# Kernel optimization log

Hardware: AMD Instinct MI355X
Metric: run time of the kernel (lower is better)

## Reference

```python
import jax, jax.numpy as jnp
import numpy as np

B, N, M = 32, 2048, 512
NUM_HEADING_BIN, NUM_SIZE_CLUSTER = 12, 8
OUT_DIM = 3 + 2 * NUM_HEADING_BIN + 4 * NUM_SIZE_CLUSTER  # 59

SPECS = [("sf_w1",64,4),("sf_w2",64,64),("sf_w3",64,64),("sf_w4",128,64),("sf_w5",1024,128),
         ("sh_w1",512,1091),("sh_w2",256,512),("sh_w3",128,256),("sh_w4",128,128),("sh_w5",2,128),
         ("t_w1",128,3),("t_w2",256,128),("t_w3",512,256),("t_fw1",256,515),("t_fw2",128,256),("t_fw3",3,128),
         ("b_w1",128,3),("b_w2",128,128),("b_w3",256,128),("b_w4",512,256),("b_fw1",512,515),("b_fw2",256,512),("b_fw3",OUT_DIM,256)]


def _bn(x, axes):
    # training-mode batch norm, gamma=1 beta=0 (fresh-init torch BatchNorm1d)
    m = jnp.mean(x, axes, keepdims=True)
    v = jnp.var(x, axes, keepdims=True)
    return (x - m) * jax.lax.rsqrt(v + 1e-5)


def _conv(x, w, b):  # 1x1 Conv1d: x (B,C,N), w (O,C), b (O,)
    return jnp.einsum('bcn,oc->bon', x, w) + b[None, :, None]


def _fc(x, w, b):  # x (B,C), w (O,C)
    return x @ w.T + b


def setup_inputs() -> dict:
    key = jax.random.key(0)
    ks = jax.random.split(key, 2 + len(SPECS))
    inp = {}
    inp["point_cloud"] = jax.random.normal(ks[0], (B, N, 4), dtype=jnp.float32)
    cls = jax.random.randint(ks[1], (B,), 0, 3)
    inp["one_hot_vec"] = jax.nn.one_hot(cls, 3, dtype=jnp.float32)
    for i, (nm, o, c) in enumerate(SPECS):
        inp[nm] = jax.random.normal(ks[2 + i], (o, c), dtype=jnp.float32) * (1.0 / np.sqrt(c))
        inp[nm.replace('w', 'b')] = jnp.zeros((o,), jnp.float32)
    return inp


def _forward(point_cloud, one_hot_vec,
             sf_w1, sf_b1, sf_w2, sf_b2, sf_w3, sf_b3, sf_w4, sf_b4, sf_w5, sf_b5,
             sh_w1, sh_b1, sh_w2, sh_b2, sh_w3, sh_b3, sh_w4, sh_b4, sh_w5, sh_b5,
             t_w1, t_b1, t_w2, t_b2, t_w3, t_b3, t_fw1, t_fb1, t_fw2, t_fb2, t_fw3, t_fb3,
             b_w1, b_b1, b_w2, b_b2, b_w3, b_b3, b_w4, b_b4, b_fw1, b_fb1, b_fw2, b_fb2, b_fw3, b_fb3):
    relu = jax.nn.relu
    Bv, Nv = point_cloud.shape[0], point_cloud.shape[1]

    # ---- PointNetSegmentation (PointNetfeat global_feat=False + seg head) ----
    x = point_cloud.transpose(0, 2, 1)                       # (B,4,N)
    h = relu(_bn(_conv(x, sf_w1, sf_b1), (0, 2)))
    pointfeat = relu(_bn(_conv(h, sf_w2, sf_b2), (0, 2)))    # (B,64,N)
    h = relu(_bn(_conv(pointfeat, sf_w3, sf_b3), (0, 2)))
    h = relu(_bn(_conv(h, sf_w4, sf_b4), (0, 2)))
    h = _bn(_conv(h, sf_w5, sf_b5), (0, 2))                  # (B,1024,N), no relu
    g = jnp.max(h, axis=2)                                   # (B,1024)
    g = jnp.concatenate([one_hot_vec, g], axis=1)            # (B,1027)
    feat = jnp.concatenate([jnp.broadcast_to(g[:, :, None], (Bv, 1027, Nv)), pointfeat], axis=1)  # (B,1091,N)
    h = relu(_bn(_conv(feat, sh_w1, sh_b1), (0, 2)))
    h = relu(_bn(_conv(h, sh_w2, sh_b2), (0, 2)))
    h = relu(_bn(_conv(h, sh_w3, sh_b3), (0, 2)))
    h = relu(_bn(_conv(h, sh_w4, sh_b4), (0, 2)))            # dropout p=0.5 -> eval identity
    logits = _conv(h, sh_w5, sh_b5).transpose(0, 2, 1)       # (B,N,2)

    # ---- point_cloud_masking: vectorized mask-select + resample-to-512 ----
    xyz = point_cloud[:, :, :3]
    mask = logits[:, :, 0] < logits[:, :, 1]                 # (B,N) bool
    cnt = jnp.sum(mask, axis=1)                              # (B,)
    mean = jnp.sum(mask[:, :, None] * xyz, axis=1) / jnp.clip(cnt, 1)[:, None].astype(xyz.dtype)
    xyz_c = xyz - mean[:, None, :]                           # centered at mask centroid
    order = jnp.argsort(jnp.logical_not(mask), axis=1, stable=True)  # masked indices first
    u = jax.random.uniform(jax.random.key(42), (Bv, M))
    pos = jnp.minimum((u * cnt[:, None].astype(u.dtype)).astype(jnp.int32),
                      jnp.maximum(cnt[:, None] - 1, 0).astype(jnp.int32))
    idx = jnp.take_along_axis(order, pos, axis=1)            # (B,M) sample w/ replacement from masked set
    object_pc = jnp.take_along_axis(xyz_c, idx[:, :, None], axis=1)  # (B,M,3)
    object_pc = jnp.where(cnt[:, None, None] > 0, object_pc, 0.0)

    x = object_pc.transpose(0, 2, 1)                         # (B,3,M)
    h = relu(_bn(_conv(x, t_w1, t_b1), (0, 2)))
    h = relu(_bn(_conv(h, t_w2, t_b2), (0, 2)))
    h = relu(_bn(_conv(h, t_w3, t_b3), (0, 2)))
    gt = jnp.max(h, axis=2)                                  # (B,512)
    gt = jnp.concatenate([one_hot_vec, gt], axis=1)          # (B,515)
    h = relu(_bn(_fc(gt, t_fw1, t_fb1), 0))
    h = relu(_bn(_fc(h, t_fw2, t_fb2), 0))
    center_delta = _fc(h, t_fw3, t_fb3)                      # (B,3)

    stage1_center = center_delta + mean
    object_pc_new = object_pc - center_delta[:, None, :]

    # ---- PointNet3DboxEstimationNet ----
    x = object_pc_new.transpose(0, 2, 1)                     # (B,3,M)
    h = relu(_bn(_conv(x, b_w1, b_b1), (0, 2)))
    h = relu(_bn(_conv(h, b_w2, b_b2), (0, 2)))
    h = relu(_bn(_conv(h, b_w3, b_b3), (0, 2)))
    h = relu(_bn(_conv(h, b_w4, b_b4), (0, 2)))
    gb = jnp.max(h, axis=2)                                  # (B,512)
    gb = jnp.concatenate([gb, one_hot_vec], axis=1)          # (B,515)
    h = relu(_bn(_fc(gb, b_fw1, b_fb1), 0))
    h = relu(_bn(_fc(h, b_fw2, b_fb2), 0))
    box_out = _fc(h, b_fw3, b_fb3)                           # (B,59)

    center = box_out[:, :3] + stage1_center                  # final box center
    return jnp.concatenate([logits.reshape(Bv, -1), box_out, center], axis=1)  # (B, 2N+59+3)


def reference(point_cloud, one_hot_vec,
              sf_w1, sf_b1, sf_w2, sf_b2, sf_w3, sf_b3, sf_w4, sf_b4, sf_w5, sf_b5,
              sh_w1, sh_b1, sh_w2, sh_b2, sh_w3, sh_b3, sh_w4, sh_b4, sh_w5, sh_b5,
              t_w1, t_b1, t_w2, t_b2, t_w3, t_b3, t_fw1, t_fb1, t_fw2, t_fb2, t_fw3, t_fb3,
              b_w1, b_b1, b_w2, b_b2, b_w3, b_b3, b_w4, b_b4, b_fw1, b_fb1, b_fw2, b_fb2, b_fw3, b_fb3):
    return _forward(point_cloud, one_hot_vec,
                    sf_w1, sf_b1, sf_w2, sf_b2, sf_w3, sf_b3, sf_w4, sf_b4, sf_w5, sf_b5,
                    sh_w1, sh_b1, sh_w2, sh_b2, sh_w3, sh_b3, sh_w4, sh_b4, sh_w5, sh_b5,
                    t_w1, t_b1, t_w2, t_b2, t_w3, t_b3, t_fw1, t_fb1, t_fw2, t_fb2, t_fw3, t_fb3,
                    b_w1, b_b1, b_w2, b_b2, b_w3, b_b3, b_w4, b_b4, b_fw1, b_fb1, b_fw2, b_fb2, b_fw3, b_fb3)
```

## Files before the change

kernel.cpp:

```cpp
#include <hip/hip_runtime.h>
#include <cstdint>


constexpr int PP   = 65536;
constexpr int PP2  = 16384;
constexpr int OUTW = 4158;

constexpr size_t F_Y1 = 0;
constexpr size_t F_Y2 = (size_t)64 * PP;
constexpr size_t F_Y3 = (size_t)128 * PP;
constexpr size_t F_Y4 = (size_t)192 * PP;
constexpr size_t F_P5S = 0;
constexpr size_t F_P5Q = (size_t)2 * 1024 * 1024;
constexpr size_t F_P5M = (size_t)128 * PP;
static_assert(F_P5Q + 2 * 1024 * 1024 <= F_Y2, "P5 partials exceed Y1 slot");
static_assert(F_P5M + 1024 * 1024 <= (size_t)192 * PP, "P5m exceeds Y3 slot");
constexpr size_t F_S1 = (size_t)320 * PP;
constexpr size_t F_S2 = 0;
constexpr size_t F_S3 = (size_t)320 * PP;
constexpr size_t F_S4 = (size_t)448 * PP;
constexpr size_t F_T1 = 0;
constexpr size_t F_T2 = F_T1 + (size_t)128 * PP2;
constexpr size_t F_PT = F_T2 + (size_t)256 * PP2;
constexpr size_t F_B1 = F_PT + (size_t)5 * 256 * 512;
constexpr size_t F_B2 = F_B1 + (size_t)128 * PP2;
constexpr size_t F_B3 = F_B2 + (size_t)128 * PP2;
constexpr size_t F_PB = F_B3 + (size_t)256 * PP2;
static_assert(F_PB + (size_t)5 * 256 * 512 <= (size_t)256 * PP, "t/b overlay overflow");
static_assert((F_PT % 2) == 0 && (F_PB % 2) == 0, "double alignment");

constexpr size_t SB       = (size_t)832 * PP;
constexpr size_t F_MASK   = SB;
constexpr size_t F_MIDX   = F_MASK + PP;
constexpr size_t F_CNT    = F_MIDX + PP;
constexpr size_t F_MEAN   = F_CNT + 32;
constexpr size_t F_GVEC   = F_MEAN + 96;
constexpr size_t F_GVT    = F_GVEC + 32 * 1027;
constexpr size_t F_GVB    = F_GVT + 32 * 515;
constexpr size_t F_GDOT   = F_GVB + 32 * 515;
constexpr size_t F_YT1    = F_GDOT + 512 * 32;
constexpr size_t F_YT2    = F_YT1 + 32 * 256;
constexpr size_t F_YB1    = F_YT2 + 32 * 128;
constexpr size_t F_YB2    = F_YB1 + 32 * 512;
constexpr size_t F_CD     = F_YB2 + 32 * 256;
constexpr size_t F_OBJ    = F_CD + 96;
constexpr size_t F_ST     = F_OBJ + (size_t)3 * PP2;
constexpr size_t F_END    = F_ST + 20 * 2048;
constexpr size_t NEED_BYTES = F_END * 4;

#define NEG_INF (-3.402823466e38f)

__global__ __launch_bounds__(256) void conv_pc_k(const float* __restrict__ pc,
                                                 const float* __restrict__ W,
                                                 const float* __restrict__ bias,
                                                 float* __restrict__ Y) {
  int p = blockIdx.x * 256 + threadIdx.x;
  int o = blockIdx.y;
  float4 v = *reinterpret_cast<const float4*>(&pc[(size_t)p * 4]);
  float s = bias[o] + v.x * W[o * 4 + 0] + v.y * W[o * 4 + 1] + v.z * W[o * 4 + 2] +
            v.w * W[o * 4 + 3];
  Y[(size_t)o * PP + p] = s;
}

__global__ __launch_bounds__(256) void conv_k3_k(const float* __restrict__ Xc,
                                                 const float* __restrict__ W,
                                                 const float* __restrict__ bias,
                                                 const float* __restrict__ cd,
                                                 float* __restrict__ Y) {
  int p = blockIdx.x * 256 + threadIdx.x;
  int o = blockIdx.y;
  int b = p >> 9;
  float x0 = Xc[p], x1 = Xc[PP2 + p], x2 = Xc[2 * PP2 + p];
  if (cd) { x0 -= cd[b * 3]; x1 -= cd[b * 3 + 1]; x2 -= cd[b * 3 + 2]; }
  Y[(size_t)o * PP2 + p] = bias[o] + x0 * W[o * 3] + x1 * W[o * 3 + 1] + x2 * W[o * 3 + 2];
}

__global__ __launch_bounds__(256) void conv_gemm_k(
    const float* __restrict__ X, int ldx, const float* __restrict__ W, int ldw, int C,
    const float* __restrict__ bias, const float* __restrict__ scale,
    const float* __restrict__ shift, int relu_in, float* __restrict__ Y, int Ptot) {
  __shared__ float Xs[16][64];
  __shared__ float Ws[64][17];
  const int tid = threadIdx.x;
  const int tx = tid & 15, ty = tid >> 4;
  const int o0 = blockIdx.x * 64, p0 = blockIdx.y * 64;
  float acc[4][4] = {};
  for (int c0 = 0; c0 < C; c0 += 16) {
#pragma unroll
    for (int j = 0; j < 4; ++j) {
      int idx = tid + j * 256;
      int k = idx >> 6, n = idx & 63;
      int c = c0 + k;
      float v = X[(size_t)c * ldx + p0 + n];
      if (scale) v = v * scale[c] + shift[c];
      if (relu_in) v = fmaxf(v, 0.f);
      Xs[k][n] = v;
    }
#pragma unroll
    for (int j = 0; j < 4; ++j) {
      int idx = tid + j * 256;
      int o = idx >> 4, k = idx & 15;
      Ws[o][k] = W[(size_t)(o0 + o) * ldw + c0 + k];
    }
    __syncthreads();
#pragma unroll
    for (int k = 0; k < 16; ++k) {
      float bx[4], aw[4];
#pragma unroll
      for (int j = 0; j < 4; ++j) bx[j] = Xs[k][tx * 4 + j];
#pragma unroll
      for (int i = 0; i < 4; ++i) aw[i] = Ws[ty * 4 + i][k];
#pragma unroll
      for (int i = 0; i < 4; ++i)
#pragma unroll
        for (int j = 0; j < 4; ++j) acc[i][j] = fmaf(aw[i], bx[j], acc[i][j]);
    }
    __syncthreads();
  }
#pragma unroll
  for (int i = 0; i < 4; ++i) {
    int o = o0 + ty * 4 + i;
    float badd = bias[o];
#pragma unroll
    for (int j = 0; j < 4; ++j) acc[i][j] += badd;
  }
#pragma unroll
  for (int i = 0; i < 4; ++i) {
    int o = o0 + ty * 4 + i;
    float4 v = make_float4(acc[i][0], acc[i][1], acc[i][2], acc[i][3]);
    *reinterpret_cast<float4*>(&Y[(size_t)o * Ptot + p0 + tx * 4]) = v;
  }
}

template <bool FUSED>
__global__ __launch_bounds__(256) void gemm_big_k(
    const float* __restrict__ X, int ldx, const float* __restrict__ W, int ldw, int C,
    const float* __restrict__ bias, const float* __restrict__ scale,
    const float* __restrict__ shift, int relu_in, const float* __restrict__ gadd,
    float* __restrict__ Y, int Ptot, double* __restrict__ psum, double* __restrict__ psq,
    float* __restrict__ pmax, int Ototal) {
  __shared__ float Xs[16][128];
  __shared__ float Wt[16][128];
  const int tid = threadIdx.x;
  const int tx = tid & 15, ty = tid >> 4;
  const int o0 = blockIdx.x * 128, p0 = blockIdx.y * 128;
  float acc[8][8] = {};
  for (int c0 = 0; c0 < C; c0 += 16) {
#pragma unroll
    for (int q = 0; q < 2; ++q) {
      int f = tid + q * 256;
      int k = f >> 5, c4 = f & 31;
      int c = c0 + k;
      float4 v = *reinterpret_cast<const float4*>(&X[(size_t)c * ldx + p0 + c4 * 4]);
      if (scale) {
        float sc = scale[c], sh = shift[c];
        v.x = v.x * sc + sh; v.y = v.y * sc + sh;
        v.z = v.z * sc + sh; v.w = v.w * sc + sh;
      }
      if (relu_in) {
        v.x = fmaxf(v.x, 0.f); v.y = fmaxf(v.y, 0.f);
        v.z = fmaxf(v.z, 0.f); v.w = fmaxf(v.w, 0.f);
      }
      *reinterpret_cast<float4*>(&Xs[k][c4 * 4]) = v;
    }
#pragma unroll
    for (int q = 0; q < 8; ++q) {
      int idx = tid + q * 256;
      int k = idx >> 7, o = idx & 127;
      Wt[k][o] = W[(size_t)(o0 + o) * ldw + c0 + k];
    }
    __syncthreads();
#pragma unroll
    for (int k = 0; k < 16; ++k) {
      float bx[8], aw[8];
      *reinterpret_cast<float4*>(&bx[0]) =
          *reinterpret_cast<const float4*>(&Xs[k][tx * 4]);
      *reinterpret_cast<float4*>(&bx[4]) =
          *reinterpret_cast<const float4*>(&Xs[k][64 + tx * 4]);
      *reinterpret_cast<float4*>(&aw[0]) =
          *reinterpret_cast<const float4*>(&Wt[k][ty * 4]);
      *reinterpret_cast<float4*>(&aw[4]) =
          *reinterpret_cast<const float4*>(&Wt[k][64 + ty * 4]);
#pragma unroll
      for (int i = 0; i < 8; ++i)
#pragma unroll
        for (int j = 0; j < 8; ++j) acc[i][j] = fmaf(aw[i], bx[j], acc[i][j]);
    }
    __syncthreads();
  }
#pragma unroll
  for (int i = 0; i < 8; ++i) {
    int ro = (i < 4) ? (ty * 4 + i) : (64 + ty * 4 + (i - 4));
    int o = o0 + ro;
    float badd = bias ? bias[o] : 0.f;
    if (gadd) badd += gadd[o * 32 + (p0 >> 11)];
#pragma unroll
    for (int j = 0; j < 8; ++j) acc[i][j] += badd;
  }
  if constexpr (!FUSED) {
#pragma unroll
    for (int i = 0; i < 8; ++i) {
      int ro = (i < 4) ? (ty * 4 + i) : (64 + ty * 4 + (i - 4));
      float* row = &Y[(size_t)(o0 + ro) * Ptot + p0];
      *reinterpret_cast<float4*>(row + tx * 4) =
          make_float4(acc[i][0], acc[i][1], acc[i][2], acc[i][3]);
      *reinterpret_cast<float4*>(row + 64 + tx * 4) =
          make_float4(acc[i][4], acc[i][5], acc[i][6], acc[i][7]);
    }
  } else {
    __shared__ double redd[16][128];
#pragma unroll
    for (int i = 0; i < 8; ++i) {
      int ro = (i < 4) ? (ty * 4 + i) : (64 + ty * 4 + (i - 4));
      double s = 0.0;
#pragma unroll
      for (int j = 0; j < 8; ++j) s += (double)acc[i][j];
      redd[tx][ro] = s;
    }
    __syncthreads();
    if (tid < 128) {
      double s = 0.0;
      for (int t = 0; t < 16; ++t) s += redd[t][tid];
      psum[(size_t)blockIdx.y * Ototal + o0 + tid] = s;
    }
    __syncthreads();
#pragma unroll
    for (int i = 0; i < 8; ++i) {
      int ro = (i < 4) ? (ty * 4 + i) : (64 + ty * 4 + (i - 4));
      double s = 0.0;
#pragma unroll
      for (int j = 0; j < 8; ++j) s += (double)acc[i][j] * (double)acc[i][j];
      redd[tx][ro] = s;
    }
    __syncthreads();
    if (tid < 128) {
      double s = 0.0;
      for (int t = 0; t < 16; ++t) s += redd[t][tid];
      psq[(size_t)blockIdx.y * Ototal + o0 + tid] = s;
    }
    __syncthreads();
#pragma unroll
    for (int i = 0; i < 8; ++i) {
      int ro = (i < 4) ? (ty * 4 + i) : (64 + ty * 4 + (i - 4));
      float mx = acc[i][0];
#pragma unroll
      for (int j = 1; j < 8; ++j) mx = fmaxf(mx, acc[i][j]);
      redd[tx][ro] = (double)mx;
    }
    __syncthreads();
    if (tid < 128) {
      double s = -1.0e300;
      for (int t = 0; t < 16; ++t) s = s > redd[t][tid] ? s : redd[t][tid];
      pmax[(size_t)blockIdx.y * Ototal + o0 + tid] = (float)s;
    }
  }
}

__global__ __launch_bounds__(256) void stats_k(const float* __restrict__ Y, int Ptot,
                                               float* __restrict__ scale,
                                               float* __restrict__ shift) {
  int o = blockIdx.x;
  const float* row = Y + (size_t)o * Ptot;
  double s = 0.0, q = 0.0;
  for (int p = threadIdx.x; p < Ptot; p += 256) {
    double v = (double)row[p];
    s += v;
    q += v * v;
  }
  __shared__ double ss[256], qq[256];
  int tid = threadIdx.x;
  ss[tid] = s; qq[tid] = q;
  __syncthreads();
  for (int off = 128; off; off >>= 1) {
    if (tid < off) { ss[tid] += ss[tid + off]; qq[tid] += qq[tid + off]; }
    __syncthreads();
  }
  if (tid == 0) {
    double m = ss[0] / (double)Ptot;
    double v = qq[0] / (double)Ptot - m * m;
    if (v < 0.0) v = 0.0;
    double sc = 1.0 / sqrt(v + 1e-5);
    scale[o] = (float)sc;
    shift[o] = (float)(-m * sc);
  }
}

__global__ void stats_reduce_k(const double* __restrict__ psum, const double* __restrict__ psq,
                               int ntiles, int O, double invP, float* __restrict__ scale,
                               float* __restrict__ shift) {
  int o = blockIdx.x * blockDim.x + threadIdx.x;
  if (o >= O) return;
  double s = 0.0, q = 0.0;
  for (int t = 0; t < ntiles; ++t) {
    s += psum[(size_t)t * O + o];
    q += psq[(size_t)t * O + o];
  }
  double m = s * invP;
  double v = q * invP - m * m;
  if (v < 0.0) v = 0.0;
  double sc = 1.0 / sqrt(v + 1e-5);
  scale[o] = (float)sc;
  shift[o] = (float)(-m * sc);
}

__global__ void maxpool_g_k(const float* __restrict__ pmax, int tilesPB, int O,
                            const float* __restrict__ scale, const float* __restrict__ shift,
                            int relu, float* __restrict__ out, int ostride, int ooff) {
  int idx = blockIdx.x * blockDim.x + threadIdx.x;
  if (idx >= 32 * O) return;
  int b = idx / O, o = idx - b * O;
  float m = NEG_INF;
  for (int t = b * tilesPB; t < (b + 1) * tilesPB; ++t) m = fmaxf(m, pmax[(size_t)t * O + o]);
  float v = scale[o] * m + shift[o];
  if (relu) v = fmaxf(v, 0.f);
  out[(size_t)b * ostride + ooff + o] = v;
}

__global__ void onehot_k(const float* __restrict__ oh, float* __restrict__ gvec,
                         float* __restrict__ gvt, float* __restrict__ gvb) {
  int i = threadIdx.x;
  if (i >= 96) return;
  int b = i / 3, c = i - b * 3;
  float v = oh[b * 3 + c];
  gvec[b * 1027 + c] = v;
  gvt[b * 515 + c] = v;
  gvb[b * 515 + 512 + c] = v;
}

__global__ void gdot_k(const float* __restrict__ W, const float* __restrict__ gvec,
                       float* __restrict__ gdot) {
  int idx = blockIdx.x * 256 + threadIdx.x;
  int o = idx >> 5, b = idx & 31;
  double s = 0.0;
  const float* wr = W + (size_t)o * 1091;
  const float* gr = gvec + (size_t)b * 1027;
  for (int c = 0; c < 1027; ++c) s += (double)wr[c] * (double)gr[c];
  gdot[o * 32 + b] = (float)s;
}

__global__ __launch_bounds__(256) void logits_k(const float* __restrict__ S4,
                                                const float* __restrict__ W,
                                                const float* __restrict__ bias,
                                                const float* __restrict__ scale,
                                                const float* __restrict__ shift,
                                                float* __restrict__ out,
                                                int* __restrict__ mask) {
  int p = blockIdx.x * 256 + threadIdx.x;
  double l0 = (double)bias[0], l1 = (double)bias[1];
  for (int c = 0; c < 128; ++c) {
    float v = fmaxf(S4[(size_t)c * PP + p] * scale[c] + shift[c], 0.f);
    l0 += (double)v * (double)W[c];
    l1 += (double)v * (double)W[128 + c];
  }
  int b = p >> 11, n = p & 2047;
  out[(size_t)b * OUTW + 2 * n] = (float)l0;
  out[(size_t)b * OUTW + 2 * n + 1] = (float)l1;
  mask[p] = (l0 < l1) ? 1 : 0;
}

__global__ __launch_bounds__(256) void compact_k(const int* __restrict__ mask,
                                                 const float* __restrict__ pc,
                                                 int* __restrict__ midx, int* __restrict__ cnt,
                                                 float* __restrict__ meanv) {
  int b = blockIdx.x, tid = threadIdx.x;
  __shared__ int sc[256];
  __shared__ int base;
  __shared__ double red[256];
  __shared__ double totals[3];
  if (tid == 0) base = 0;
  __syncthreads();
  double sx = 0.0, sy = 0.0, sz = 0.0;
  for (int n0 = 0; n0 < 2048; n0 += 256) {
    int n = n0 + tid;
    int mval = mask[b * 2048 + n];
    sc[tid] = mval;
    __syncthreads();
    for (int off = 1; off < 256; off <<= 1) {
      int v = (tid >= off) ? sc[tid - off] : 0;
      __syncthreads();
      sc[tid] += v;
      __syncthreads();
    }
    int excl = sc[tid] - mval;
    if (mval) {
      midx[b * 2048 + base + excl] = n;
      const float* q = &pc[((size_t)(b * 2048 + n)) * 4];
      sx += (double)q[0]; sy += (double)q[1]; sz += (double)q[2];
    }
    __syncthreads();
    if (tid == 0) base += sc[255];
    __syncthreads();
  }
  red[tid] = sx; __syncthreads();
  for (int off = 128; off; off >>= 1) { if (tid < off) red[tid] += red[tid + off]; __syncthreads(); }
  if (tid == 0) totals[0] = red[0];
  __syncthreads();
  red[tid] = sy; __syncthreads();
  for (int off = 128; off; off >>= 1) { if (tid < off) red[tid] += red[tid + off]; __syncthreads(); }
  if (tid == 0) totals[1] = red[0];
  __syncthreads();
  red[tid] = sz; __syncthreads();
  for (int off = 128; off; off >>= 1) { if (tid < off) red[tid] += red[tid + off]; __syncthreads(); }
  if (tid == 0) {
    totals[2] = red[0];
    int c = base;
    cnt[b] = c;
    double d = (double)(c > 1 ? c : 1);
    meanv[b * 3 + 0] = (float)(totals[0] / d);
    meanv[b * 3 + 1] = (float)(totals[1] / d);
    meanv[b * 3 + 2] = (float)(totals[2] / d);
  }
}

__device__ __forceinline__ uint32_t rotl32(uint32_t x, int r) {
  return (x << r) | (x >> (32 - r));
}
__device__ inline void threefry2x32(uint32_t k0, uint32_t k1, uint32_t& x0, uint32_t& x1) {
  const uint32_t ks[3] = {k0, k1, k0 ^ k1 ^ 0x1BD11BDAu};
  const int rot[2][4] = {{13, 15, 26, 6}, {17, 29, 16, 24}};
  x0 += ks[0]; x1 += ks[1];
  for (int i = 0; i < 5; ++i) {
    const int* r = rot[i & 1];
    for (int j = 0; j < 4; ++j) {
      x0 += x1; x1 = rotl32(x1, r[j]); x1 ^= x0;
    }
    x0 += ks[(i + 1) % 3];
    x1 += ks[(i + 2) % 3] + (uint32_t)(i + 1);
  }
}

__global__ void sample_k(const float* __restrict__ pc, const int* __restrict__ midx,
                         const int* __restrict__ cnt, const float* __restrict__ meanv,
                         float* __restrict__ obj) {
  int e = blockIdx.x * 256 + threadIdx.x;
  if (e >= 16384) return;
  uint32_t x0 = 0u, x1 = (uint32_t)e;
  threefry2x32(0u, 42u, x0, x1);
  uint32_t bits = x0 ^ x1;
  float u = __uint_as_float((bits >> 9) | 0x3F800000u) - 1.0f;
  int b = e >> 9;
  int m = e & 511;
  int c_ = cnt[b];
  int pos = (int)(u * (float)c_);
  int cap = c_ - 1; if (cap < 0) cap = 0;
  if (pos > cap) pos = cap;
  float vx = 0.f, vy = 0.f, vz = 0.f;
  if (c_ > 0) {
    int n = midx[b * 2048 + pos];
    const float* q = &pc[((size_t)(b * 2048 + n)) * 4];
    vx = q[0] - meanv[b * 3 + 0];
    vy = q[1] - meanv[b * 3 + 1];
    vz = q[2] - meanv[b * 3 + 2];
  }
  int p2 = b * 512 + m;
  obj[p2] = vx;
  obj[PP2 + p2] = vy;
  obj[2 * PP2 + p2] = vz;
}

__global__ void fc_gemm_k(const float* __restrict__ Xf, int ldx, int K,
                          const float* __restrict__ W, const float* __restrict__ bias,
                          const float* __restrict__ scale, const float* __restrict__ shift,
                          int relu, float* __restrict__ Y, int ldy, int yoff, int O) {
  int o = blockIdx.x * blockDim.x + threadIdx.x;
  int b = blockIdx.y;
  if (o >= O) return;
  const float* x = Xf + (size_t)b * ldx;
  const float* w = W + (size_t)o * K;
  double s = bias ? (double)bias[o] : 0.0;
  for (int k = 0; k < K; ++k) {
    float v = x[k];
    if (scale) {
      v = v * scale[k] + shift[k];
      if (relu) v = fmaxf(v, 0.f);
    }
    s += (double)v * (double)w[k];
  }
  Y[(size_t)b * ldy + yoff + o] = (float)s;
}

__global__ void fc_stats_k(const float* __restrict__ Y, int ldy, int O,
                           float* __restrict__ scale, float* __restrict__ shift) {
  int o = blockIdx.x * blockDim.x + threadIdx.x;
  if (o >= O) return;
  double s = 0.0, q = 0.0;
  for (int b = 0; b < 32; ++b) {
    double v = (double)Y[(size_t)b * ldy + o];
    s += v;
    q += v * v;
  }
  double m = s / 32.0;
  double v = q / 32.0 - m * m;
  if (v < 0.0) v = 0.0;
  double sc = 1.0 / sqrt(v + 1e-5);
  scale[o] = (float)sc;
  shift[o] = (float)(-m * sc);
}

__global__ void center_k(float* __restrict__ out, const float* __restrict__ cd,
                         const float* __restrict__ meanv) {
  int i = threadIdx.x;
  if (i >= 96) return;
  int b = i / 3, c = i - b * 3;
  out[(size_t)b * OUTW + 4155 + c] =
      out[(size_t)b * OUTW + 4096 + c] + cd[b * 3 + c] + meanv[b * 3 + c];
}

__global__ void size_fail_k(float* out, float code) {
  if (threadIdx.x == 0 && blockIdx.x == 0) out[0] = code;
}

extern "C" void kernel_launch(void* const* d_in, const int* in_sizes, int n_in, void* d_out,
                              int out_size, void* d_ws, size_t ws_size, hipStream_t stream) {
  float* out = (float*)d_out;
  static const int EXP[48] = {
      262144, 96, 256, 64, 4096, 64, 4096, 64, 8192, 128, 131072, 1024,
      558592, 512, 131072, 256, 32768, 128, 16384, 128, 256, 2,
      384, 128, 32768, 256, 131072, 512, 131840, 256, 32768, 128, 384, 3,
      384, 128, 16384, 128, 32768, 256, 131072, 512, 263680, 512, 131072, 256,
      15104, 59};
  if (n_in != 48) { size_fail_k<<<1, 1, 0, stream>>>(out, 9.0e6f + 99.0f * 1e4f); return; }
  if (out_size != 133056) { size_fail_k<<<1, 1, 0, stream>>>(out, 9.0e6f + 98.0f * 1e4f); return; }
  for (int i = 0; i < 48; ++i)
    if (in_sizes[i] != EXP[i]) {
      size_fail_k<<<1, 1, 0, stream>>>(out, 9.0e6f + (float)i * 1e4f);
      return;
    }
  if (ws_size < NEED_BYTES) { size_fail_k<<<1, 1, 0, stream>>>(out, 9.0e6f + 97.0f * 1e4f); return; }

  const float* pc = (const float*)d_in[0];
  const float* oh = (const float*)d_in[1];
#define IN(i) ((const float*)d_in[i])
  float* ws = (float*)d_ws;
  auto SC = [&](int s) { return ws + F_ST + (size_t)s * 2048; };
  auto SH = [&](int s) { return ws + F_ST + (size_t)s * 2048 + 1024; };
  enum { L_C1, L_C2, L_C3, L_C4, L_C5, L_S1, L_S2, L_S3, L_S4, L_T1, L_T2, L_T3,
         L_B1, L_B2, L_B3, L_B4, L_FT1, L_FT2, L_FB1, L_FB2 };

  float* Y1 = ws + F_Y1;
  float* Y2 = ws + F_Y2;
  float* Y3 = ws + F_Y3;
  float* Y4 = ws + F_Y4;
  double* P5s = (double*)(ws + F_P5S);
  double* P5q = (double*)(ws + F_P5Q);
  float*  P5m = ws + F_P5M;
  float* S1 = ws + F_S1;
  float* S2 = ws + F_S2;
  float* S3 = ws + F_S3;
  float* S4 = ws + F_S4;
  int* mask = (int*)(ws + F_MASK);
  int* midx = (int*)(ws + F_MIDX);
  int* cnt = (int*)(ws + F_CNT);
  float* meanv = ws + F_MEAN;
  float* gvec = ws + F_GVEC;
  float* gvt = ws + F_GVT;
  float* gvb = ws + F_GVB;
  float* gdot = ws + F_GDOT;
  float* obj = ws + F_OBJ;
  float* T1 = ws + F_T1;
  float* T2 = ws + F_T2;
  float* Bb1 = ws + F_B1;
  float* Bb2 = ws + F_B2;
  float* Bb3 = ws + F_B3;
  double* PTs = (double*)(ws + F_PT);
  double* PTq = (double*)(ws + F_PT + (size_t)2 * 256 * 512);
  float*  PTm = ws + F_PT + (size_t)4 * 256 * 512;
  double* PBs = (double*)(ws + F_PB);
  double* PBq = (double*)(ws + F_PB + (size_t)2 * 256 * 512);
  float*  PBm = ws + F_PB + (size_t)4 * 256 * 512;
  float* yt1 = ws + F_YT1;
  float* yt2 = ws + F_YT2;
  float* yb1 = ws + F_YB1;
  float* yb2 = ws + F_YB2;
  float* cd = ws + F_CD;

  dim3 blk(256);
  conv_pc_k<<<dim3(PP / 256, 64), blk, 0, stream>>>(pc, IN(2), IN(3), Y1);
  stats_k<<<64, blk, 0, stream>>>(Y1, PP, SC(L_C1), SH(L_C1));
  conv_gemm_k<<<dim3(1, PP / 64), blk, 0, stream>>>(Y1, PP, IN(4), 64, 64, IN(5),
      SC(L_C1), SH(L_C1), 1, Y2, PP);
  stats_k<<<64, blk, 0, stream>>>(Y2, PP, SC(L_C2), SH(L_C2));
  conv_gemm_k<<<dim3(1, PP / 64), blk, 0, stream>>>(Y2, PP, IN(6), 64, 64, IN(7),
      SC(L_C2), SH(L_C2), 1, Y3, PP);
  stats_k<<<64, blk, 0, stream>>>(Y3, PP, SC(L_C3), SH(L_C3));
  gemm_big_k<false><<<dim3(1, PP / 128), blk, 0, stream>>>(Y3, PP, IN(8), 64, 64, IN(9),
      SC(L_C3), SH(L_C3), 1, nullptr, Y4, PP, nullptr, nullptr, nullptr, 0);
  stats_k<<<128, blk, 0, stream>>>(Y4, PP, SC(L_C4), SH(L_C4));
  gemm_big_k<true><<<dim3(8, PP / 128), blk, 0, stream>>>(Y4, PP, IN(10), 128, 128, IN(11),
      SC(L_C4), SH(L_C4), 1, nullptr, nullptr, PP, P5s, P5q, P5m, 1024);
  stats_reduce_k<<<4, blk, 0, stream>>>(P5s, P5q, PP / 128, 1024, 1.0 / PP, SC(L_C5),
                                        SH(L_C5));
  onehot_k<<<1, 96, 0, stream>>>(oh, gvec, gvt, gvb);
  maxpool_g_k<<<(32 * 1024) / 256, blk, 0, stream>>>(P5m, 16, 1024, SC(L_C5), SH(L_C5), 0,
                                                     gvec, 1027, 3);
  gdot_k<<<64, blk, 0, stream>>>(IN(12), gvec, gdot);
  gemm_big_k<false><<<dim3(4, PP / 128), blk, 0, stream>>>(Y2, PP, IN(12) + 1027, 1091, 64,
      IN(13), SC(L_C2), SH(L_C2), 1, gdot, S1, PP, nullptr, nullptr, nullptr, 0);
  stats_k<<<512, blk, 0, stream>>>(S1, PP, SC(L_S1), SH(L_S1));
  gemm_big_k<false><<<dim3(2, PP / 128), blk, 0, stream>>>(S1, PP, IN(14), 512, 512, IN(15),
      SC(L_S1), SH(L_S1), 1, nullptr, S2, PP, nullptr, nullptr, nullptr, 0);
  stats_k<<<256, blk, 0, stream>>>(S2, PP, SC(L_S2), SH(L_S2));
  gemm_big_k<false><<<dim3(1, PP / 128), blk, 0, stream>>>(S2, PP, IN(16), 256, 256, IN(17),
      SC(L_S2), SH(L_S2), 1, nullptr, S3, PP, nullptr, nullptr, nullptr, 0);
  stats_k<<<128, blk, 0, stream>>>(S3, PP, SC(L_S3), SH(L_S3));
  gemm_big_k<false><<<dim3(1, PP / 128), blk, 0, stream>>>(S3, PP, IN(18), 128, 128, IN(19),
      SC(L_S3), SH(L_S3), 1, nullptr, S4, PP, nullptr, nullptr, nullptr, 0);
  stats_k<<<128, blk, 0, stream>>>(S4, PP, SC(L_S4), SH(L_S4));
  logits_k<<<PP / 256, blk, 0, stream>>>(S4, IN(20), IN(21), SC(L_S4), SH(L_S4), out, mask);
  compact_k<<<32, blk, 0, stream>>>(mask, pc, midx, cnt, meanv);
  sample_k<<<64, blk, 0, stream>>>(pc, midx, cnt, meanv, obj);
  conv_k3_k<<<dim3(PP2 / 256, 128), blk, 0, stream>>>(obj, IN(22), IN(23), nullptr, T1);
  stats_k<<<128, blk, 0, stream>>>(T1, PP2, SC(L_T1), SH(L_T1));
  gemm_big_k<false><<<dim3(2, PP2 / 128), blk, 0, stream>>>(T1, PP2, IN(24), 128, 128,
      IN(25), SC(L_T1), SH(L_T1), 1, nullptr, T2, PP2, nullptr, nullptr, nullptr, 0);
  stats_k<<<256, blk, 0, stream>>>(T2, PP2, SC(L_T2), SH(L_T2));
  gemm_big_k<true><<<dim3(4, PP2 / 128), blk, 0, stream>>>(T2, PP2, IN(26), 256, 256,
      IN(27), SC(L_T2), SH(L_T2), 1, nullptr, nullptr, PP2, PTs, PTq, PTm, 512);
  stats_reduce_k<<<2, blk, 0, stream>>>(PTs, PTq, PP2 / 128, 512, 1.0 / PP2, SC(L_T3),
                                        SH(L_T3));
  maxpool_g_k<<<(32 * 512) / 256, blk, 0, stream>>>(PTm, 4, 512, SC(L_T3), SH(L_T3), 1, gvt,
                                                    515, 3);
  fc_gemm_k<<<dim3(1, 32), blk, 0, stream>>>(gvt, 515, 515, IN(28), IN(29), nullptr, nullptr,
                                             0, yt1, 256, 0, 256);
  fc_stats_k<<<1, blk, 0, stream>>>(yt1, 256, 256, SC(L_FT1), SH(L_FT1));
  fc_gemm_k<<<dim3(1, 32), blk, 0, stream>>>(yt1, 256, 256, IN(30), IN(31), SC(L_FT1),
                                             SH(L_FT1), 1, yt2, 128, 0, 128);
  fc_stats_k<<<1, blk, 0, stream>>>(yt2, 128, 128, SC(L_FT2), SH(L_FT2));
  fc_gemm_k<<<dim3(1, 32), blk, 0, stream>>>(yt2, 128, 128, IN(32), IN(33), SC(L_FT2),
                                             SH(L_FT2), 1, cd, 3, 0, 3);
  conv_k3_k<<<dim3(PP2 / 256, 128), blk, 0, stream>>>(obj, IN(34), IN(35), cd, Bb1);
  stats_k<<<128, blk, 0, stream>>>(Bb1, PP2, SC(L_B1), SH(L_B1));
  gemm_big_k<false><<<dim3(1, PP2 / 128), blk, 0, stream>>>(Bb1, PP2, IN(36), 128, 128,
      IN(37), SC(L_B1), SH(L_B1), 1, nullptr, Bb2, PP2, nullptr, nullptr, nullptr, 0);
  stats_k<<<128, blk, 0, stream>>>(Bb2, PP2, SC(L_B2), SH(L_B2));
  gemm_big_k<false><<<dim3(2, PP2 / 128), blk, 0, stream>>>(Bb2, PP2, IN(38), 128, 128,
      IN(39), SC(L_B2), SH(L_B2), 1, nullptr, Bb3, PP2, nullptr, nullptr, nullptr, 0);
  stats_k<<<256, blk, 0, stream>>>(Bb3, PP2, SC(L_B3), SH(L_B3));
  gemm_big_k<true><<<dim3(4, PP2 / 128), blk, 0, stream>>>(Bb3, PP2, IN(40), 256, 256,
      IN(41), SC(L_B3), SH(L_B3), 1, nullptr, nullptr, PP2, PBs, PBq, PBm, 512);
  stats_reduce_k<<<2, blk, 0, stream>>>(PBs, PBq, PP2 / 128, 512, 1.0 / PP2, SC(L_B4),
                                        SH(L_B4));
  maxpool_g_k<<<(32 * 512) / 256, blk, 0, stream>>>(PBm, 4, 512, SC(L_B4), SH(L_B4), 1, gvb,
                                                    515, 0);
  fc_gemm_k<<<dim3(2, 32), blk, 0, stream>>>(gvb, 515, 515, IN(42), IN(43), nullptr, nullptr,
                                             0, yb1, 512, 0, 512);
  fc_stats_k<<<2, blk, 0, stream>>>(yb1, 512, 512, SC(L_FB1), SH(L_FB1));
  fc_gemm_k<<<dim3(1, 32), blk, 0, stream>>>(yb1, 512, 512, IN(44), IN(45), SC(L_FB1),
                                             SH(L_FB1), 1, yb2, 256, 0, 256);
  fc_stats_k<<<1, blk, 0, stream>>>(yb2, 256, 256, SC(L_FB2), SH(L_FB2));
  fc_gemm_k<<<dim3(1, 32), blk, 0, stream>>>(yb2, 256, 256, IN(46), IN(47), SC(L_FB2),
                                             SH(L_FB2), 1, out, OUTW, 4096, 59);
  center_k<<<1, 96, 0, stream>>>(out, cd, meanv);
#undef IN
}
```

Measured before the change: 2.393 ms.

## Fuse batch-norm statistics into GEMM epilogues instead of separate stats passes

Adds a GEMM mode that writes the output and also emits per-tile double-precision sum and sum-of-squares partials. Each later stats_reduce_k combines these partials into scale and shift. This replaces the separate stats_k passes that re-read full activation tensors (up to 512 channels by 65536 points) after most big conv layers. The cost is extra shared-memory reductions and syncs in each GEMM epilogue, plus workspace overlays that must not collide with live buffers.

```diff
diff --git a/kernel.cpp b/kernel.cpp
--- a/kernel.cpp
+++ b/kernel.cpp
@@ -19,6 +19,10 @@
 constexpr size_t F_S2 = 0;
 constexpr size_t F_S3 = (size_t)320 * PP;
 constexpr size_t F_S4 = (size_t)448 * PP;
+constexpr size_t F_PA_C4 = 0;
+constexpr size_t F_PA_S1 = (size_t)128 * PP;
+constexpr size_t F_PA_S2 = (size_t)256 * PP;
+constexpr size_t F_PA_TB = (size_t)448 * PP;
 constexpr size_t F_T1 = 0;
 constexpr size_t F_T2 = F_T1 + (size_t)128 * PP2;
 constexpr size_t F_PT = F_T2 + (size_t)256 * PP2;
@@ -132,7 +136,7 @@
   }
 }
 
-template <bool FUSED>
+template <int MODE>
 __global__ __launch_bounds__(256) void gemm_big_k(
     const float* __restrict__ X, int ldx, const float* __restrict__ W, int ldw, int C,
     const float* __restrict__ bias, const float* __restrict__ scale,
@@ -197,7 +201,7 @@
 #pragma unroll
     for (int j = 0; j < 8; ++j) acc[i][j] += badd;
   }
-  if constexpr (!FUSED) {
+  if constexpr (MODE != 2) {
 #pragma unroll
     for (int i = 0; i < 8; ++i) {
       int ro = (i < 4) ? (ty * 4 + i) : (64 + ty * 4 + (i - 4));
@@ -207,7 +211,8 @@
       *reinterpret_cast<float4*>(row + 64 + tx * 4) =
           make_float4(acc[i][4], acc[i][5], acc[i][6], acc[i][7]);
     }
-  } else {
+  }
+  if constexpr (MODE >= 1) {
     __shared__ double redd[16][128];
 #pragma unroll
     for (int i = 0; i < 8; ++i) {
@@ -238,20 +243,22 @@
       for (int t = 0; t < 16; ++t) s += redd[t][tid];
       psq[(size_t)blockIdx.y * Ototal + o0 + tid] = s;
     }
-    __syncthreads();
-#pragma unroll
-    for (int i = 0; i < 8; ++i) {
-      int ro = (i < 4) ? (ty * 4 + i) : (64 + ty * 4 + (i - 4));
-      float mx = acc[i][0];
-#pragma unroll
-      for (int j = 1; j < 8; ++j) mx = fmaxf(mx, acc[i][j]);
-      redd[tx][ro] = (double)mx;
-    }
-    __syncthreads();
-    if (tid < 128) {
-      double s = -1.0e300;
-      for (int t = 0; t < 16; ++t) s = s > redd[t][tid] ? s : redd[t][tid];
-      pmax[(size_t)blockIdx.y * Ototal + o0 + tid] = (float)s;
+    if constexpr (MODE == 2) {
+      __syncthreads();
+#pragma unroll
+      for (int i = 0; i < 8; ++i) {
+        int ro = (i < 4) ? (ty * 4 + i) : (64 + ty * 4 + (i - 4));
+        float mx = acc[i][0];
+#pragma unroll
+        for (int j = 1; j < 8; ++j) mx = fmaxf(mx, acc[i][j]);
+        redd[tx][ro] = (double)mx;
+      }
+      __syncthreads();
+      if (tid < 128) {
+        double s = -1.0e300;
+        for (int t = 0; t < 16; ++t) s = s > redd[t][tid] ? s : redd[t][tid];
+        pmax[(size_t)blockIdx.y * Ototal + o0 + tid] = (float)s;
+      }
     }
   }
 }
@@ -573,8 +580,14 @@
   float* yb1 = ws + F_YB1;
   float* yb2 = ws + F_YB2;
   float* cd = ws + F_CD;
+  double* PAc4 = (double*)(ws + F_PA_C4);
+  double* PAs1 = (double*)(ws + F_PA_S1);
+  double* PAs  = (double*)(ws + F_PA_S2);
+  double* PAtb = (double*)(ws + F_PA_TB);
 
   dim3 blk(256);
+  const int NT  = PP / 128;
+  const int NT2 = PP2 / 128;
   conv_pc_k<<<dim3(PP / 256, 64), blk, 0, stream>>>(pc, IN(2), IN(3), Y1);
   stats_k<<<64, blk, 0, stream>>>(Y1, PP, SC(L_C1), SH(L_C1));
   conv_gemm_k<<<dim3(1, PP / 64), blk, 0, stream>>>(Y1, PP, IN(4), 64, 64, IN(5),
@@ -583,41 +596,47 @@
   conv_gemm_k<<<dim3(1, PP / 64), blk, 0, stream>>>(Y2, PP, IN(6), 64, 64, IN(7),
       SC(L_C2), SH(L_C2), 1, Y3, PP);
   stats_k<<<64, blk, 0, stream>>>(Y3, PP, SC(L_C3), SH(L_C3));
-  gemm_big_k<false><<<dim3(1, PP / 128), blk, 0, stream>>>(Y3, PP, IN(8), 64, 64, IN(9),
-      SC(L_C3), SH(L_C3), 1, nullptr, Y4, PP, nullptr, nullptr, nullptr, 0);
-  stats_k<<<128, blk, 0, stream>>>(Y4, PP, SC(L_C4), SH(L_C4));
-  gemm_big_k<true><<<dim3(8, PP / 128), blk, 0, stream>>>(Y4, PP, IN(10), 128, 128, IN(11),
+  gemm_big_k<1><<<dim3(1, NT), blk, 0, stream>>>(Y3, PP, IN(8), 64, 64, IN(9),
+      SC(L_C3), SH(L_C3), 1, nullptr, Y4, PP, PAc4, PAc4 + (size_t)NT * 128, nullptr, 128);
+  stats_reduce_k<<<1, blk, 0, stream>>>(PAc4, PAc4 + (size_t)NT * 128, NT, 128, 1.0 / PP,
+                                        SC(L_C4), SH(L_C4));
+  gemm_big_k<2><<<dim3(8, NT), blk, 0, stream>>>(Y4, PP, IN(10), 128, 128, IN(11),
       SC(L_C4), SH(L_C4), 1, nullptr, nullptr, PP, P5s, P5q, P5m, 1024);
-  stats_reduce_k<<<4, blk, 0, stream>>>(P5s, P5q, PP / 128, 1024, 1.0 / PP, SC(L_C5),
-                                        SH(L_C5));
+  stats_reduce_k<<<4, blk, 0, stream>>>(P5s, P5q, NT, 1024, 1.0 / PP, SC(L_C5), SH(L_C5));
   onehot_k<<<1, 96, 0, stream>>>(oh, gvec, gvt, gvb);
   maxpool_g_k<<<(32 * 1024) / 256, blk, 0, stream>>>(P5m, 16, 1024, SC(L_C5), SH(L_C5), 0,
                                                      gvec, 1027, 3);
   gdot_k<<<64, blk, 0, stream>>>(IN(12), gvec, gdot);
-  gemm_big_k<false><<<dim3(4, PP / 128), blk, 0, stream>>>(Y2, PP, IN(12) + 1027, 1091, 64,
-      IN(13), SC(L_C2), SH(L_C2), 1, gdot, S1, PP, nullptr, nullptr, nullptr, 0);
-  stats_k<<<512, blk, 0, stream>>>(S1, PP, SC(L_S1), SH(L_S1));
-  gemm_big_k<false><<<dim3(2, PP / 128), blk, 0, stream>>>(S1, PP, IN(14), 512, 512, IN(15),
-      SC(L_S1), SH(L_S1), 1, nullptr, S2, PP, nullptr, nullptr, nullptr, 0);
-  stats_k<<<256, blk, 0, stream>>>(S2, PP, SC(L_S2), SH(L_S2));
-  gemm_big_k<false><<<dim3(1, PP / 128), blk, 0, stream>>>(S2, PP, IN(16), 256, 256, IN(17),
-      SC(L_S2), SH(L_S2), 1, nullptr, S3, PP, nullptr, nullptr, nullptr, 0);
-  stats_k<<<128, blk, 0, stream>>>(S3, PP, SC(L_S3), SH(L_S3));
-  gemm_big_k<false><<<dim3(1, PP / 128), blk, 0, stream>>>(S3, PP, IN(18), 128, 128, IN(19),
-      SC(L_S3), SH(L_S3), 1, nullptr, S4, PP, nullptr, nullptr, nullptr, 0);
-  stats_k<<<128, blk, 0, stream>>>(S4, PP, SC(L_S4), SH(L_S4));
+  gemm_big_k<1><<<dim3(4, NT), blk, 0, stream>>>(Y2, PP, IN(12) + 1027, 1091, 64,
+      IN(13), SC(L_C2), SH(L_C2), 1, gdot, S1, PP, PAs1, PAs1 + (size_t)NT * 512, nullptr,
+      512);
+  stats_reduce_k<<<2, blk, 0, stream>>>(PAs1, PAs1 + (size_t)NT * 512, NT, 512, 1.0 / PP,
+                                        SC(L_S1), SH(L_S1));
+  gemm_big_k<1><<<dim3(2, NT), blk, 0, stream>>>(S1, PP, IN(14), 512, 512, IN(15),
+      SC(L_S1), SH(L_S1), 1, nullptr, S2, PP, PAs, PAs + (size_t)NT * 256, nullptr, 256);
+  stats_reduce_k<<<1, blk, 0, stream>>>(PAs, PAs + (size_t)NT * 256, NT, 256, 1.0 / PP,
+                                        SC(L_S2), SH(L_S2));
+  gemm_big_k<1><<<dim3(1, NT), blk, 0, stream>>>(S2, PP, IN(16), 256, 256, IN(17),
+      SC(L_S2), SH(L_S2), 1, nullptr, S3, PP, PAs, PAs + (size_t)NT * 128, nullptr, 128);
+  stats_reduce_k<<<1, blk, 0, stream>>>(PAs, PAs + (size_t)NT * 128, NT, 128, 1.0 / PP,
+                                        SC(L_S3), SH(L_S3));
+  gemm_big_k<1><<<dim3(1, NT), blk, 0, stream>>>(S3, PP, IN(18), 128, 128, IN(19),
+      SC(L_S3), SH(L_S3), 1, nullptr, S4, PP, PAs, PAs + (size_t)NT * 128, nullptr, 128);
+  stats_reduce_k<<<1, blk, 0, stream>>>(PAs, PAs + (size_t)NT * 128, NT, 128, 1.0 / PP,
+                                        SC(L_S4), SH(L_S4));
   logits_k<<<PP / 256, blk, 0, stream>>>(S4, IN(20), IN(21), SC(L_S4), SH(L_S4), out, mask);
   compact_k<<<32, blk, 0, stream>>>(mask, pc, midx, cnt, meanv);
   sample_k<<<64, blk, 0, stream>>>(pc, midx, cnt, meanv, obj);
   conv_k3_k<<<dim3(PP2 / 256, 128), blk, 0, stream>>>(obj, IN(22), IN(23), nullptr, T1);
   stats_k<<<128, blk, 0, stream>>>(T1, PP2, SC(L_T1), SH(L_T1));
-  gemm_big_k<false><<<dim3(2, PP2 / 128), blk, 0, stream>>>(T1, PP2, IN(24), 128, 128,
-      IN(25), SC(L_T1), SH(L_T1), 1, nullptr, T2, PP2, nullptr, nullptr, nullptr, 0);
-  stats_k<<<256, blk, 0, stream>>>(T2, PP2, SC(L_T2), SH(L_T2));
-  gemm_big_k<true><<<dim3(4, PP2 / 128), blk, 0, stream>>>(T2, PP2, IN(26), 256, 256,
+  gemm_big_k<1><<<dim3(2, NT2), blk, 0, stream>>>(T1, PP2, IN(24), 128, 128,
+      IN(25), SC(L_T1), SH(L_T1), 1, nullptr, T2, PP2, PAtb, PAtb + (size_t)NT2 * 256,
+      nullptr, 256);
+  stats_reduce_k<<<1, blk, 0, stream>>>(PAtb, PAtb + (size_t)NT2 * 256, NT2, 256, 1.0 / PP2,
+                                        SC(L_T2), SH(L_T2));
+  gemm_big_k<2><<<dim3(4, NT2), blk, 0, stream>>>(T2, PP2, IN(26), 256, 256,
       IN(27), SC(L_T2), SH(L_T2), 1, nullptr, nullptr, PP2, PTs, PTq, PTm, 512);
-  stats_reduce_k<<<2, blk, 0, stream>>>(PTs, PTq, PP2 / 128, 512, 1.0 / PP2, SC(L_T3),
-                                        SH(L_T3));
+  stats_reduce_k<<<2, blk, 0, stream>>>(PTs, PTq, NT2, 512, 1.0 / PP2, SC(L_T3), SH(L_T3));
   maxpool_g_k<<<(32 * 512) / 256, blk, 0, stream>>>(PTm, 4, 512, SC(L_T3), SH(L_T3), 1, gvt,
                                                     515, 3);
   fc_gemm_k<<<dim3(1, 32), blk, 0, stream>>>(gvt, 515, 515, IN(28), IN(29), nullptr, nullptr,
@@ -630,16 +649,19 @@
                                              SH(L_FT2), 1, cd, 3, 0, 3);
   conv_k3_k<<<dim3(PP2 / 256, 128), blk, 0, stream>>>(obj, IN(34), IN(35), cd, Bb1);
   stats_k<<<128, blk, 0, stream>>>(Bb1, PP2, SC(L_B1), SH(L_B1));
-  gemm_big_k<false><<<dim3(1, PP2 / 128), blk, 0, stream>>>(Bb1, PP2, IN(36), 128, 128,
-      IN(37), SC(L_B1), SH(L_B1), 1, nullptr, Bb2, PP2, nullptr, nullptr, nullptr, 0);
-  stats_k<<<128, blk, 0, stream>>>(Bb2, PP2, SC(L_B2), SH(L_B2));
-  gemm_big_k<false><<<dim3(2, PP2 / 128), blk, 0, stream>>>(Bb2, PP2, IN(38), 128, 128,
-      IN(39), SC(L_B2), SH(L_B2), 1, nullptr, Bb3, PP2, nullptr, nullptr, nullptr, 0);
-  stats_k<<<256, blk, 0, stream>>>(Bb3, PP2, SC(L_B3), SH(L_B3));
-  gemm_big_k<true><<<dim3(4, PP2 / 128), blk, 0, stream>>>(Bb3, PP2, IN(40), 256, 256,
+  gemm_big_k<1><<<dim3(1, NT2), blk, 0, stream>>>(Bb1, PP2, IN(36), 128, 128,
+      IN(37), SC(L_B1), SH(L_B1), 1, nullptr, Bb2, PP2, PAtb, PAtb + (size_t)NT2 * 128,
+      nullptr, 128);
+  stats_reduce_k<<<1, blk, 0, stream>>>(PAtb, PAtb + (size_t)NT2 * 128, NT2, 128, 1.0 / PP2,
+                                        SC(L_B2), SH(L_B2));
+  gemm_big_k<1><<<dim3(2, NT2), blk, 0, stream>>>(Bb2, PP2, IN(38), 128, 128,
+      IN(39), SC(L_B2), SH(L_B2), 1, nullptr, Bb3, PP2, PAtb, PAtb + (size_t)NT2 * 256,
+      nullptr, 256);
+  stats_reduce_k<<<1, blk, 0, stream>>>(PAtb, PAtb + (size_t)NT2 * 256, NT2, 256, 1.0 / PP2,
+                                        SC(L_B3), SH(L_B3));
+  gemm_big_k<2><<<dim3(4, NT2), blk, 0, stream>>>(Bb3, PP2, IN(40), 256, 256,
       IN(41), SC(L_B3), SH(L_B3), 1, nullptr, nullptr, PP2, PBs, PBq, PBm, 512);
-  stats_reduce_k<<<2, blk, 0, stream>>>(PBs, PBq, PP2 / 128, 512, 1.0 / PP2, SC(L_B4),
-                                        SH(L_B4));
+  stats_reduce_k<<<2, blk, 0, stream>>>(PBs, PBq, NT2, 512, 1.0 / PP2, SC(L_B4), SH(L_B4));
   maxpool_g_k<<<(32 * 512) / 256, blk, 0, stream>>>(PBm, 4, 512, SC(L_B4), SH(L_B4), 1, gvb,
                                                     515, 0);
   fc_gemm_k<<<dim3(2, 32), blk, 0, stream>>>(gvb, 515, 515, IN(42), IN(43), nullptr, nullptr,
```

After: 2.854 ms. 1.19x slower.
